# Kernel optimization log

Hardware: AMD Instinct MI355X
Metric: run time of the kernel (lower is better)

## Reference

```python
import jax, jax.numpy as jnp
import numpy as np

G = 2048   # geneNum
E = 512    # emb_len
B = 16     # batch


def setup_inputs() -> dict:
    key = jax.random.key(0)
    ks = jax.random.split(key, 12)
    xav = 1.0 / np.sqrt(2.0)  # xavier gain used in reset_parameters

    def xavier(k, shape, gain):
        fan_in, fan_out = shape[1], shape[0]
        a = gain * np.sqrt(6.0 / (fan_in + fan_out))
        return jax.random.uniform(k, shape, jnp.float32, -a, a)

    return {
        "datax": jax.random.randint(ks[0], (B, G), 0, 5),
        "embMat": jax.random.normal(ks[1], (G, E), jnp.float32),      # frozen embedding table
        "Wq": xavier(ks[2], (E, E), xav),
        "Wk": xavier(ks[3], (E, E), xav),
        "k1": jax.random.normal(ks[4], (G, G), jnp.float32),
        "k2": jax.random.normal(ks[5], (G, G), jnp.float32),
        "k3": jax.random.normal(ks[6], (1,), jnp.float32),
        "shortestPath": jax.random.randint(ks[7], (G, G), 1, 8).astype(jnp.float32),
        "centralityMat": jax.random.uniform(ks[8], (G, G), jnp.float32),
        "padding": (jax.random.uniform(ks[9], (G, G)) > 0.1).astype(jnp.float32),
        "fc1_w": xavier(ks[10], (G, G), xav),
        "fc1_b": jnp.zeros((G,), jnp.float32),
        "fcCox_w": xavier(ks[11], (1, G), xav),
    }


def reference(datax, embMat, Wq, Wk, k1, k2, k3, shortestPath,
              centralityMat, padding, fc1_w, fc1_b, fcCox_w):
    # In torch, originalx aliases x, so the in-place binarization makes the
    # embedding indices binary (0/1).
    xbin = (datax != 0).astype(jnp.int32)          # [B, G]
    originalx = xbin.astype(jnp.float32)           # [B, G]
    x = embMat[xbin]                               # [B, G, E] (rows 0/1 of table)

    q = jnp.einsum('bge,fe->bgf', x, Wq)           # Linear no-bias: x @ Wq.T
    k = jnp.einsum('bge,fe->bgf', x, Wk)

    attn_weights = jnp.einsum('bge,bhe->bgh', q, k)  # [B, G, G]
    lrelu = lambda t: jax.nn.leaky_relu(t, 0.01)
    bias = (lrelu(k1) * shortestPath
            + lrelu(k2) * centralityMat
            + lrelu(k3) * padding)                 # [G, G]
    attn_weights = attn_weights + bias
    attn_weights_origin = attn_weights

    aw = jax.nn.softmax(attn_weights, axis=-1)     # [B, G, G]
    v = (datax != 0).astype(jnp.float32)           # binary values, [B, G]
    attn = jnp.einsum('bgh,bh->bg', aw, v)         # bmm with [B,G,1] + squeeze
    # Dropout(p=0.2) -> identity (eval / deterministic baseline)
    attn = originalx + attn
    attn = attn @ fc1_w.T + fc1_b                  # fc1
    output = attn @ fcCox_w.T                      # [B, 1]
    return output.reshape(-1), attn_weights_origin
```

## Files before the change

### kernel.cpp

```cpp
#include <hip/hip_runtime.h>
#include <stdint.h>

#define GN 2048
#define EN 512
#define BN 16

__device__ __forceinline__ float bf2f(unsigned short u) {
    return __uint_as_float(((unsigned int)u) << 16);
}
__device__ __forceinline__ unsigned short f2bf(float f) {
    unsigned int u = __float_as_uint(f);
    u += 0x7fffu + ((u >> 16) & 1u);
    return (unsigned short)(u >> 16);
}
__device__ __forceinline__ float lrelu(float v) { return v > 0.f ? v : 0.01f * v; }

union U16x8 { uint4 v; unsigned short s[8]; };

template<bool ISBF>
__device__ __forceinline__ float ldf(const void* p, size_t i) {
    if (ISBF) return bf2f(((const unsigned short*)p)[i]);
    return ((const float*)p)[i];
}

template<bool ISBF>
__device__ __forceinline__ void ld8(const void* p, size_t off, float* v) {
    if (ISBF) {
        U16x8 u; u.v = *(const uint4*)((const unsigned short*)p + off);
        #pragma unroll
        for (int i = 0; i < 8; i++) v[i] = bf2f(u.s[i]);
    } else {
        const float* q = (const float*)p + off;
        const float4 a = *(const float4*)q;
        const float4 b = *(const float4*)(q + 4);
        v[0]=a.x; v[1]=a.y; v[2]=a.z; v[3]=a.w;
        v[4]=b.x; v[5]=b.y; v[6]=b.z; v[7]=b.w;
    }
}

__global__ void sniff_k(const unsigned int* __restrict__ emb, int* __restrict__ flag) {
    const int t = threadIdx.x;
    const unsigned int w = emb[t];
    const int e = (w >> 7) & 0xFF;
    const int ok = (e >= 108 && e <= 134) ? 1 : 0;
    const unsigned long long m = __ballot(ok);
    if (t == 0) flag[0] = (__popcll(m) >= 40) ? 1 : 0;
}

template<bool ISBF>
__device__ __forceinline__ void setup_body(
    const int* __restrict__ datax, const void* emb, const void* Wq, const void* Wk,
    const void* fc1w, const void* fcCox,
    unsigned char* __restrict__ xpackT, float* __restrict__ qk,
    float* __restrict__ partials)
{
    const int blk = blockIdx.x;
    const int t = threadIdx.x;

    if (blk < 16) {
        const int b = blk;
        unsigned int byte = 0;
        const int base = b * GN + t * 8;
        #pragma unroll
        for (int i = 0; i < 8; i++)
            byte |= (datax[base + i] != 0 ? 1u : 0u) << i;
        xpackT[t * 16 + b] = (unsigned char)byte;
    } else if (blk < 272) {
        const int iw = (blk - 16) * 4 + (t >> 6);
        const int lane = t & 63;
        const void* W = (iw < 512) ? Wq : Wk;
        const int f = iw & 511;
        float w8[8], e0[8], e1[8];
        ld8<ISBF>(W, (size_t)f * EN + lane * 8, w8);
        ld8<ISBF>(emb, (size_t)lane * 8, e0);
        ld8<ISBF>(emb, (size_t)EN + lane * 8, e1);
        float d0 = 0.f, d1 = 0.f;
        #pragma unroll
        for (int i = 0; i < 8; i++) { d0 += w8[i] * e0[i]; d1 += w8[i] * e1[i]; }
        for (int o = 32; o >= 1; o >>= 1) {
            d0 += __shfl_xor(d0, o);
            d1 += __shfl_xor(d1, o);
        }
        if (lane == 0) {
            const int base = (iw < 512) ? 0 : 1024;
            qk[base + f] = d0;
            qk[base + 512 + f] = d1;
        }
    } else {
        const int pb = blk - 272;
        float acc[8] = {0.f,0.f,0.f,0.f,0.f,0.f,0.f,0.f};
        for (int r = 0; r < 16; r++) {
            const int g = pb * 16 + r;
            const float c = ldf<ISBF>(fcCox, g);
            float w8[8];
            ld8<ISBF>(fc1w, (size_t)g * GN + t * 8, w8);
            #pragma unroll
            for (int i = 0; i < 8; i++) acc[i] += c * w8[i];
        }
        float* q = partials + (size_t)pb * GN + t * 8;
        *(float4*)q       = make_float4(acc[0], acc[1], acc[2], acc[3]);
        *(float4*)(q + 4) = make_float4(acc[4], acc[5], acc[6], acc[7]);
    }
}

__global__ __launch_bounds__(256) void setup_k(
    const int* datax, const void* emb, const void* Wq, const void* Wk,
    const void* fc1w, const void* fcCox,
    unsigned char* xpackT, float* qk, float* partials, const int* flag)
{
    if (flag[0]) setup_body<true>(datax, emb, Wq, Wk, fc1w, fcCox, xpackT, qk, partials);
    else         setup_body<false>(datax, emb, Wq, Wk, fc1w, fcCox, xpackT, qk, partials);
}

template<bool ISBF>
__device__ __forceinline__ void pre2_body(
    const float* __restrict__ qk, const void* fc1b, const void* fcCox,
    const float* __restrict__ partials,
    float* __restrict__ sv, float* __restrict__ cptr, float* __restrict__ weff)
{
    const int t = threadIdx.x;
    if (blockIdx.x > 0) {
        const int c = (blockIdx.x - 1) * 256 + t;
        float acc = 0.f;
        for (int r = 0; r < 128; r++)
            acc += partials[(size_t)r * GN + c];
        weff[c] = acc;
        return;
    }
    float a[5] = {0.f, 0.f, 0.f, 0.f, 0.f};
    for (int e = t; e < EN; e += 256) {
        float q0 = qk[e], q1 = qk[EN + e];
        float K0 = qk[2 * EN + e], K1 = qk[3 * EN + e];
        a[0] += q0 * K0; a[1] += q0 * K1; a[2] += q1 * K0; a[3] += q1 * K1;
    }
    for (int gg = t; gg < GN; gg += 256)
        a[4] += ldf<ISBF>(fc1b, gg) * ldf<ISBF>(fcCox, gg);
    for (int o = 32; o >= 1; o >>= 1)
        #pragma unroll
        for (int j = 0; j < 5; j++) a[j] += __shfl_xor(a[j], o);
    __shared__ float red[4][5];
    int wid = t >> 6, lane = t & 63;
    if (lane == 0)
        for (int j = 0; j < 5; j++) red[wid][j] = a[j];
    __syncthreads();
    if (t == 0) {
        for (int j = 0; j < 4; j++)
            sv[j] = red[0][j] + red[1][j] + red[2][j] + red[3][j];
        cptr[0] = red[0][4] + red[1][4] + red[2][4] + red[3][4];
    }
}

__global__ __launch_bounds__(256) void pre2_k(
    const float* qk, const void* fc1b, const void* fcCox, const float* partials,
    float* sv, float* cptr, float* weff, const int* flag)
{
    if (flag[0]) pre2_body<true>(qk, fc1b, fcCox, partials, sv, cptr, weff);
    else         pre2_body<false>(qk, fc1b, fcCox, partials, sv, cptr, weff);
}

template<bool ISBF>
__device__ __forceinline__ void attn_body(
    const void* k1, const void* k2, const void* k3,
    const void* sp, const void* cen, const void* pad,
    const unsigned char* __restrict__ xpackT, const float* __restrict__ sv,
    float* __restrict__ attn2, void* d_out)
{
    const int g = blockIdx.x;
    const int t = threadIdx.x;
    const int h0 = t << 3;
    const size_t roff = (size_t)g * GN + h0;

    const float lr3 = lrelu(ldf<ISBF>(k3, 0));

    float a1[8], a2[8], vsp[8], vcn[8], vpd[8];
    ld8<ISBF>(k1, roff, a1);
    ld8<ISBF>(k2, roff, a2);
    ld8<ISBF>(sp, roff, vsp);
    ld8<ISBF>(cen, roff, vcn);
    ld8<ISBF>(pad, roff, vpd);

    float bias8[8];
    float lmax = -3.4e38f;
    #pragma unroll
    for (int i = 0; i < 8; i++) {
        float b = lrelu(a1[i]) * vsp[i] + lrelu(a2[i]) * vcn[i] + lr3 * vpd[i];
        bias8[i] = b;
        lmax = fmaxf(lmax, b);
    }
    for (int o = 32; o >= 1; o >>= 1) lmax = fmaxf(lmax, __shfl_xor(lmax, o));

    __shared__ float smax[4];
    __shared__ float redT[4];
    __shared__ float red[4][BN];
    const int wid = t >> 6, lane = t & 63;
    if (lane == 0) smax[wid] = lmax;
    __syncthreads();
    const float Mg = fmaxf(fmaxf(smax[0], smax[1]), fmaxf(smax[2], smax[3]));

    float E8[8];
    float Tl = 0.f;
    #pragma unroll
    for (int i = 0; i < 8; i++) { E8[i] = __expf(bias8[i] - Mg); Tl += E8[i]; }

    const uint4 pk = *(const uint4*)(xpackT + (size_t)t * 16);
    const unsigned char* pb = (const unsigned char*)&pk;

    float s1l[BN];
    #pragma unroll
    for (int b = 0; b < BN; b++) {
        const unsigned int mk = pb[b];
        float acc1 = 0.f;
        #pragma unroll
        for (int i = 0; i < 8; i++)
            acc1 += ((mk >> i) & 1u) ? E8[i] : 0.f;
        s1l[b] = acc1;
    }
    for (int o = 32; o >= 1; o >>= 1) {
        Tl += __shfl_xor(Tl, o);
        #pragma unroll
        for (int b = 0; b < BN; b++) s1l[b] += __shfl_xor(s1l[b], o);
    }
    if (lane == 0) {
        redT[wid] = Tl;
        #pragma unroll
        for (int b = 0; b < BN; b++) red[wid][b] = s1l[b];
    }
    __syncthreads();

    const float s00 = sv[0], s01 = sv[1], s10 = sv[2], s11 = sv[3];
    const uint4 gk = *(const uint4*)(xpackT + (size_t)(g >> 3) * 16);
    const unsigned char* gb = (const unsigned char*)&gk;
    const int gbit = g & 7;

    if (t < BN) {
        const int b = t;
        const float Tg = redT[0] + redT[1] + redT[2] + redT[3];
        const float S1 = fmaxf(red[0][b] + red[1][b] + red[2][b] + red[3][b], 1e-30f);
        const float S0 = fmaxf(Tg - S1, 1e-30f);
        const bool on = ((gb[b] >> gbit) & 1u) != 0u;
        const float sa0 = on ? s10 : s00;
        const float sa1 = on ? s11 : s01;
        const float d = (sa0 + __logf(S0)) - (sa1 + __logf(S1));
        const float attnv = 1.f / (1.f + __expf(d));
        attn2[b * GN + g] = (on ? 1.f : 0.f) + attnv;
    }

    const int brot = g & 15;
    if (ISBF) {
        U16x8 p00, p01, p10, p11;
        #pragma unroll
        for (int i = 0; i < 8; i++) {
            p00.s[i] = f2bf(bias8[i] + s00);
            p01.s[i] = f2bf(bias8[i] + s01);
            p10.s[i] = f2bf(bias8[i] + s10);
            p11.s[i] = f2bf(bias8[i] + s11);
        }
        unsigned short* outp = (unsigned short*)d_out + BN + (size_t)g * GN + h0;
        #pragma unroll
        for (int bb = 0; bb < BN; bb++) {
            const int b = (bb + brot) & 15;
            const unsigned int mk = pb[b];
            const bool on = ((gb[b] >> gbit) & 1u) != 0u;
            U16x8 lo, hi;
            if (on) { lo = p10; hi = p11; } else { lo = p00; hi = p01; }
            U16x8 o;
            #pragma unroll
            for (int i = 0; i < 8; i++)
                o.s[i] = ((mk >> i) & 1u) ? hi.s[i] : lo.s[i];
            *(uint4*)(outp + (size_t)b * GN * GN) = o.v;
        }
    } else {
        float v00[8], v01[8], v10[8], v11[8];
        #pragma unroll
        for (int i = 0; i < 8; i++) {
            v00[i] = bias8[i] + s00;
            v01[i] = bias8[i] + s01;
            v10[i] = bias8[i] + s10;
            v11[i] = bias8[i] + s11;
        }
        float* outp = (float*)d_out + BN + (size_t)g * GN + h0;
        #pragma unroll
        for (int bb = 0; bb < BN; bb++) {
            const int b = (bb + brot) & 15;
            const unsigned int mk = pb[b];
            const bool on = ((gb[b] >> gbit) & 1u) != 0u;
            float ov[8];
            #pragma unroll
            for (int i = 0; i < 8; i++) {
                const float lo = on ? v10[i] : v00[i];
                const float hi = on ? v11[i] : v01[i];
                ov[i] = ((mk >> i) & 1u) ? hi : lo;
            }
            float* q = outp + (size_t)b * GN * GN;
            *(float4*)q       = make_float4(ov[0], ov[1], ov[2], ov[3]);
            *(float4*)(q + 4) = make_float4(ov[4], ov[5], ov[6], ov[7]);
        }
    }
}

__global__ __launch_bounds__(256) void attn_k(
    const void* k1, const void* k2, const void* k3,
    const void* sp, const void* cen, const void* pad,
    const unsigned char* xpackT, const float* sv, float* attn2,
    void* d_out, const int* flag)
{
    if (flag[0]) attn_body<true>(k1, k2, k3, sp, cen, pad, xpackT, sv, attn2, d_out);
    else         attn_body<false>(k1, k2, k3, sp, cen, pad, xpackT, sv, attn2, d_out);
}

template<bool ISBF>
__device__ __forceinline__ void final_body(
    const float* __restrict__ attn2, const float* __restrict__ weff,
    const float* __restrict__ cptr, void* d_out)
{
    const int b = blockIdx.x, t = threadIdx.x;
    const int h0 = t << 3;
    const float4 a0 = *(const float4*)(attn2 + b * GN + h0);
    const float4 a1 = *(const float4*)(attn2 + b * GN + h0 + 4);
    const float4 w0 = *(const float4*)(weff + h0);
    const float4 w1 = *(const float4*)(weff + h0 + 4);
    float acc = a0.x * w0.x + a0.y * w0.y + a0.z * w0.z + a0.w * w0.w
              + a1.x * w1.x + a1.y * w1.y + a1.z * w1.z + a1.w * w1.w;
    for (int o = 32; o >= 1; o >>= 1) acc += __shfl_xor(acc, o);
    __shared__ float red[4];
    const int wid = t >> 6, lane = t & 63;
    if (lane == 0) red[wid] = acc;
    __syncthreads();
    if (t == 0) {
        const float val = cptr[0] + red[0] + red[1] + red[2] + red[3];
        if (ISBF) ((unsigned short*)d_out)[b] = f2bf(val);
        else      ((float*)d_out)[b] = val;
    }
}

__global__ __launch_bounds__(256) void final_k(
    const float* attn2, const float* weff, const float* cptr,
    void* d_out, const int* flag)
{
    if (flag[0]) final_body<true>(attn2, weff, cptr, d_out);
    else         final_body<false>(attn2, weff, cptr, d_out);
}

extern "C" void kernel_launch(void* const* d_in, const int* in_sizes, int n_in,
                              void* d_out, int out_size, void* d_ws, size_t ws_size,
                              hipStream_t stream) {
    const int*  datax = (const int*)d_in[0];
    const void* emb   = d_in[1];
    const void* Wq    = d_in[2];
    const void* Wk    = d_in[3];
    const void* k1    = d_in[4];
    const void* k2    = d_in[5];
    const void* k3    = d_in[6];
    const void* sp    = d_in[7];
    const void* cen   = d_in[8];
    const void* pad   = d_in[9];
    const void* fc1w  = d_in[10];
    const void* fc1b  = d_in[11];
    const void* fcCox = d_in[12];

    float* ws       = (float*)d_ws;
    float* qk       = ws;
    float* sv       = ws + 2048;
    float* cptr     = ws + 2052;
    float* weff     = ws + 2056;
    float* attn2    = ws + 4104;
    float* partials = ws + 36872;
    unsigned char* xpackT = (unsigned char*)(ws + 299016);
    int*   flag     = (int*)(ws + 300040);

    sniff_k<<<1, 64, 0, stream>>>((const unsigned int*)emb, flag);
    setup_k<<<400, 256, 0, stream>>>(datax, emb, Wq, Wk, fc1w, fcCox,
                                     xpackT, qk, partials, flag);
    pre2_k<<<9, 256, 0, stream>>>(qk, fc1b, fcCox, partials, sv, cptr, weff, flag);
    attn_k<<<GN, 256, 0, stream>>>(k1, k2, k3, sp, cen, pad, xpackT, sv, attn2, d_out, flag);
    final_k<<<BN, 256, 0, stream>>>(attn2, weff, cptr, d_out, flag);
}
```

Baseline: 408.1 us.

## Process four attention rows per block and swizzle block-to-row mapping

The attention kernel now handles four consecutive g rows per block (512 blocks instead of 2048), batching the bias loads, reductions and shuffles across rows and writing four output rows per batch. Block indices are permuted so neighbouring blocks cover distant row groups, and byte extraction from packed masks uses register shifts instead of byte-addressed local arrays. This aims to cut per-block overhead, syncs and local-memory spills, at the cost of more registers (s1l[4][16], bias[4][8]) and less occupancy. The kernel is dominated by writing the 16×G×G output, so the gain is limited.

```diff
diff --git a/kernel.cpp b/kernel.cpp
--- a/kernel.cpp
+++ b/kernel.cpp
@@ -16,6 +16,13 @@
 __device__ __forceinline__ float lrelu(float v) { return v > 0.f ? v : 0.01f * v; }
 
 union U16x8 { uint4 v; unsigned short s[8]; };
+
+__device__ __forceinline__ unsigned int byte_of(const uint4& v, int b) {
+    const unsigned long long lo = ((unsigned long long)v.y << 32) | v.x;
+    const unsigned long long hi = ((unsigned long long)v.w << 32) | v.z;
+    const unsigned long long sel = (b & 8) ? hi : lo;
+    return (unsigned int)(sel >> ((b & 7) * 8)) & 0xFFu;
+}
 
 template<bool ISBF>
 __device__ __forceinline__ float ldf(const void* p, size_t i) {
@@ -165,135 +172,158 @@
     const unsigned char* __restrict__ xpackT, const float* __restrict__ sv,
     float* __restrict__ attn2, void* d_out)
 {
-    const int g = blockIdx.x;
-    const int t = threadIdx.x;
-    const int h0 = t << 3;
-    const size_t roff = (size_t)g * GN + h0;
+    const int id  = blockIdx.x;
+    const int idp = ((id & 7) << 6) | (id >> 3);
+    const int G0  = idp << 2;
+    const int t   = threadIdx.x;
+    const int h0  = t << 3;
 
     const float lr3 = lrelu(ldf<ISBF>(k3, 0));
 
-    float a1[8], a2[8], vsp[8], vcn[8], vpd[8];
-    ld8<ISBF>(k1, roff, a1);
-    ld8<ISBF>(k2, roff, a2);
-    ld8<ISBF>(sp, roff, vsp);
-    ld8<ISBF>(cen, roff, vcn);
-    ld8<ISBF>(pad, roff, vpd);
-
-    float bias8[8];
-    float lmax = -3.4e38f;
+    float bias[4][8];
+    float lmax[4];
     #pragma unroll
-    for (int i = 0; i < 8; i++) {
-        float b = lrelu(a1[i]) * vsp[i] + lrelu(a2[i]) * vcn[i] + lr3 * vpd[i];
-        bias8[i] = b;
-        lmax = fmaxf(lmax, b);
-    }
-    for (int o = 32; o >= 1; o >>= 1) lmax = fmaxf(lmax, __shfl_xor(lmax, o));
-
-    __shared__ float smax[4];
-    __shared__ float redT[4];
-    __shared__ float red[4][BN];
+    for (int r = 0; r < 4; r++) {
+        const size_t roff = (size_t)(G0 + r) * GN + h0;
+        float a1[8], a2[8], vsp[8], vcn[8], vpd[8];
+        ld8<ISBF>(k1, roff, a1);
+        ld8<ISBF>(k2, roff, a2);
+        ld8<ISBF>(sp, roff, vsp);
+        ld8<ISBF>(cen, roff, vcn);
+        ld8<ISBF>(pad, roff, vpd);
+        float lm = -3.4e38f;
+        #pragma unroll
+        for (int i = 0; i < 8; i++) {
+            float b = lrelu(a1[i]) * vsp[i] + lrelu(a2[i]) * vcn[i] + lr3 * vpd[i];
+            bias[r][i] = b;
+            lm = fmaxf(lm, b);
+        }
+        lmax[r] = lm;
+    }
+    #pragma unroll
+    for (int o = 32; o >= 1; o >>= 1)
+        #pragma unroll
+        for (int r = 0; r < 4; r++) lmax[r] = fmaxf(lmax[r], __shfl_xor(lmax[r], o));
+
+    __shared__ float smax[4][4];
+    __shared__ float redT[4][4];
+    __shared__ float red[4][4][BN];
     const int wid = t >> 6, lane = t & 63;
-    if (lane == 0) smax[wid] = lmax;
+    if (lane == 0)
+        #pragma unroll
+        for (int r = 0; r < 4; r++) smax[wid][r] = lmax[r];
     __syncthreads();
-    const float Mg = fmaxf(fmaxf(smax[0], smax[1]), fmaxf(smax[2], smax[3]));
-
-    float E8[8];
-    float Tl = 0.f;
+    float Mg[4];
     #pragma unroll
-    for (int i = 0; i < 8; i++) { E8[i] = __expf(bias8[i] - Mg); Tl += E8[i]; }
+    for (int r = 0; r < 4; r++)
+        Mg[r] = fmaxf(fmaxf(smax[0][r], smax[1][r]), fmaxf(smax[2][r], smax[3][r]));
 
     const uint4 pk = *(const uint4*)(xpackT + (size_t)t * 16);
-    const unsigned char* pb = (const unsigned char*)&pk;
-
-    float s1l[BN];
+
+    float Tl[4], s1l[4][BN];
     #pragma unroll
-    for (int b = 0; b < BN; b++) {
-        const unsigned int mk = pb[b];
-        float acc1 = 0.f;
-        #pragma unroll
-        for (int i = 0; i < 8; i++)
-            acc1 += ((mk >> i) & 1u) ? E8[i] : 0.f;
-        s1l[b] = acc1;
-    }
+    for (int r = 0; r < 4; r++) {
+        float E8[8]; float T = 0.f;
+        #pragma unroll
+        for (int i = 0; i < 8; i++) { E8[i] = __expf(bias[r][i] - Mg[r]); T += E8[i]; }
+        Tl[r] = T;
+        #pragma unroll
+        for (int b = 0; b < BN; b++) {
+            const unsigned int mk = byte_of(pk, b);
+            float acc = 0.f;
+            #pragma unroll
+            for (int i = 0; i < 8; i++) acc += ((mk >> i) & 1u) ? E8[i] : 0.f;
+            s1l[r][b] = acc;
+        }
+    }
+    #pragma unroll
     for (int o = 32; o >= 1; o >>= 1) {
-        Tl += __shfl_xor(Tl, o);
-        #pragma unroll
-        for (int b = 0; b < BN; b++) s1l[b] += __shfl_xor(s1l[b], o);
+        #pragma unroll
+        for (int r = 0; r < 4; r++) {
+            Tl[r] += __shfl_xor(Tl[r], o);
+            #pragma unroll
+            for (int b = 0; b < BN; b++) s1l[r][b] += __shfl_xor(s1l[r][b], o);
+        }
     }
     if (lane == 0) {
-        redT[wid] = Tl;
-        #pragma unroll
-        for (int b = 0; b < BN; b++) red[wid][b] = s1l[b];
+        #pragma unroll
+        for (int r = 0; r < 4; r++) {
+            redT[wid][r] = Tl[r];
+            #pragma unroll
+            for (int b = 0; b < BN; b++) red[wid][r][b] = s1l[r][b];
+        }
     }
     __syncthreads();
 
     const float s00 = sv[0], s01 = sv[1], s10 = sv[2], s11 = sv[3];
-    const uint4 gk = *(const uint4*)(xpackT + (size_t)(g >> 3) * 16);
-    const unsigned char* gb = (const unsigned char*)&gk;
-    const int gbit = g & 7;
-
-    if (t < BN) {
-        const int b = t;
-        const float Tg = redT[0] + redT[1] + redT[2] + redT[3];
-        const float S1 = fmaxf(red[0][b] + red[1][b] + red[2][b] + red[3][b], 1e-30f);
+    const uint4 gk = *(const uint4*)(xpackT + (size_t)(G0 >> 3) * 16);
+    const int gsh = G0 & 7;
+
+    if (t < 64) {
+        const int b = t & 15, r = t >> 4;
+        const float Tg = redT[0][r] + redT[1][r] + redT[2][r] + redT[3][r];
+        const float S1 = fmaxf(red[0][r][b] + red[1][r][b] + red[2][r][b] + red[3][r][b], 1e-30f);
         const float S0 = fmaxf(Tg - S1, 1e-30f);
-        const bool on = ((gb[b] >> gbit) & 1u) != 0u;
+        const bool on = ((byte_of(gk, b) >> (gsh + r)) & 1u) != 0u;
         const float sa0 = on ? s10 : s00;
         const float sa1 = on ? s11 : s01;
         const float d = (sa0 + __logf(S0)) - (sa1 + __logf(S1));
         const float attnv = 1.f / (1.f + __expf(d));
-        attn2[b * GN + g] = (on ? 1.f : 0.f) + attnv;
-    }
-
-    const int brot = g & 15;
+        attn2[b * GN + (G0 + r)] = (on ? 1.f : 0.f) + attnv;
+    }
+
+    const int prot = idp & 15;
     if (ISBF) {
-        U16x8 p00, p01, p10, p11;
-        #pragma unroll
-        for (int i = 0; i < 8; i++) {
-            p00.s[i] = f2bf(bias8[i] + s00);
-            p01.s[i] = f2bf(bias8[i] + s01);
-            p10.s[i] = f2bf(bias8[i] + s10);
-            p11.s[i] = f2bf(bias8[i] + s11);
-        }
-        unsigned short* outp = (unsigned short*)d_out + BN + (size_t)g * GN + h0;
+        U16x8 p00[4], p01[4], p10[4], p11[4];
+        #pragma unroll
+        for (int r = 0; r < 4; r++)
+            #pragma unroll
+            for (int i = 0; i < 8; i++) {
+                p00[r].s[i] = f2bf(bias[r][i] + s00);
+                p01[r].s[i] = f2bf(bias[r][i] + s01);
+                p10[r].s[i] = f2bf(bias[r][i] + s10);
+                p11[r].s[i] = f2bf(bias[r][i] + s11);
+            }
+        unsigned short* outp = (unsigned short*)d_out + BN + h0;
         #pragma unroll
         for (int bb = 0; bb < BN; bb++) {
-            const int b = (bb + brot) & 15;
-            const unsigned int mk = pb[b];
-            const bool on = ((gb[b] >> gbit) & 1u) != 0u;
-            U16x8 lo, hi;
-            if (on) { lo = p10; hi = p11; } else { lo = p00; hi = p01; }
-            U16x8 o;
-            #pragma unroll
-            for (int i = 0; i < 8; i++)
-                o.s[i] = ((mk >> i) & 1u) ? hi.s[i] : lo.s[i];
-            *(uint4*)(outp + (size_t)b * GN * GN) = o.v;
+            const int b = (bb + prot) & 15;
+            const unsigned int mk = byte_of(pk, b);
+            const unsigned int gbyte = byte_of(gk, b);
+            unsigned short* bp = outp + (size_t)b * GN * GN;
+            #pragma unroll
+            for (int r = 0; r < 4; r++) {
+                const bool on = ((gbyte >> (gsh + r)) & 1u) != 0u;
+                U16x8 lo, hi;
+                if (on) { lo = p10[r]; hi = p11[r]; } else { lo = p00[r]; hi = p01[r]; }
+                U16x8 o;
+                #pragma unroll
+                for (int i = 0; i < 8; i++)
+                    o.s[i] = ((mk >> i) & 1u) ? hi.s[i] : lo.s[i];
+                *(uint4*)(bp + (size_t)(G0 + r) * GN) = o.v;
+            }
         }
     } else {
-        float v00[8], v01[8], v10[8], v11[8];
-        #pragma unroll
-        for (int i = 0; i < 8; i++) {
-            v00[i] = bias8[i] + s00;
-            v01[i] = bias8[i] + s01;
-            v10[i] = bias8[i] + s10;
-            v11[i] = bias8[i] + s11;
-        }
-        float* outp = (float*)d_out + BN + (size_t)g * GN + h0;
+        float* outp = (float*)d_out + BN + h0;
         #pragma unroll
         for (int bb = 0; bb < BN; bb++) {
-            const int b = (bb + brot) & 15;
-            const unsigned int mk = pb[b];
-            const bool on = ((gb[b] >> gbit) & 1u) != 0u;
-            float ov[8];
-            #pragma unroll
-            for (int i = 0; i < 8; i++) {
-                const float lo = on ? v10[i] : v00[i];
-                const float hi = on ? v11[i] : v01[i];
-                ov[i] = ((mk >> i) & 1u) ? hi : lo;
+            const int b = (bb + prot) & 15;
+            const unsigned int mk = byte_of(pk, b);
+            const unsigned int gbyte = byte_of(gk, b);
+            float* bp = outp + (size_t)b * GN * GN;
+            #pragma unroll
+            for (int r = 0; r < 4; r++) {
+                const bool on = ((gbyte >> (gsh + r)) & 1u) != 0u;
+                const float c0 = on ? s10 : s00;
+                const float c1 = on ? s11 : s01;
+                float ov[8];
+                #pragma unroll
+                for (int i = 0; i < 8; i++)
+                    ov[i] = bias[r][i] + (((mk >> i) & 1u) ? c1 : c0);
+                float* q = bp + (size_t)(G0 + r) * GN;
+                *(float4*)q       = make_float4(ov[0], ov[1], ov[2], ov[3]);
+                *(float4*)(q + 4) = make_float4(ov[4], ov[5], ov[6], ov[7]);
             }
-            float* q = outp + (size_t)b * GN * GN;
-            *(float4*)q       = make_float4(ov[0], ov[1], ov[2], ov[3]);
-            *(float4*)(q + 4) = make_float4(ov[4], ov[5], ov[6], ov[7]);
         }
     }
 }
@@ -372,6 +402,6 @@
     setup_k<<<400, 256, 0, stream>>>(datax, emb, Wq, Wk, fc1w, fcCox,
                                      xpackT, qk, partials, flag);
     pre2_k<<<9, 256, 0, stream>>>(qk, fc1b, fcCox, partials, sv, cptr, weff, flag);
-    attn_k<<<GN, 256, 0, stream>>>(k1, k2, k3, sp, cen, pad, xpackT, sv, attn2, d_out, flag);
+    attn_k<<<512, 256, 0, stream>>>(k1, k2, k3, sp, cen, pad, xpackT, sv, attn2, d_out, flag);
     final_k<<<BN, 256, 0, stream>>>(attn2, weff, cptr, d_out, flag);
 }
```

After: 397.5 us. 2.6% less time.
